# Performance work log

Hardware: AMD Instinct MI355X
Metric: run time of the kernel (lower is better)

## Reference

```python
import jax, jax.numpy as jnp
import numpy as np

B, TE, TD, E, H, V, A, MAXOOV = 8, 400, 100, 128, 256, 50000, 612, 50
VEXT = V + MAXOOV


def setup_inputs():
    key = jax.random.key(0)
    it = iter(jax.random.split(key, 40))
    def nrm(shape, s=0.05):
        return jax.random.normal(next(it), shape, jnp.float32) * s
    inp = {
        "encoder_tokens": jax.random.randint(next(it), (B, TE), 0, V, dtype=jnp.int32),
        "decoder_tokens": jax.random.randint(next(it), (B, TD), 0, V, dtype=jnp.int32),
        "encoder_ext_tokens": jax.random.randint(next(it), (B, TE), 0, VEXT, dtype=jnp.int32),
        "encoder_mask": jnp.ones((B, TE), jnp.float32),
        "embedding": nrm((V, E)),
        "Wih_f": nrm((E, 4 * H)), "Whh_f": nrm((H, 4 * H)), "b_f": jnp.zeros((4 * H,), jnp.float32),
        "Wih_b": nrm((E, 4 * H)), "Whh_b": nrm((H, 4 * H)), "b_b": jnp.zeros((4 * H,), jnp.float32),
        "Wred": nrm((2 * H, H)), "bred": jnp.zeros((H,), jnp.float32),
        "Wenc_feat": nrm((2 * H, A)), "benc_feat": jnp.zeros((A,), jnp.float32),
        "v": nrm((A,), 1.0),
        "Wx": nrm((E + 2 * H, E)), "bx": jnp.zeros((E,), jnp.float32),
        "Wih_d": nrm((E, 4 * H)), "Whh_d": nrm((H, 4 * H)), "b_d": jnp.zeros((4 * H,), jnp.float32),
        "Wdf": nrm((TD, 2 * H, A)), "bdf": jnp.zeros((TD, A), jnp.float32),
        "Wpg": nrm((2 * H + H + H + E, 1)), "bpg": jnp.zeros((1,), jnp.float32),
        "Wout": nrm((H + 2 * H, H)), "bout": jnp.zeros((H,), jnp.float32),
        "Wv": nrm((H, V)), "bv": jnp.zeros((V,), jnp.float32),
    }
    return inp


def _lstm(xs, Wih, Whh, b):
    # xs: [T, B, E] -> outputs [T, B, H], final (h, c)
    def step(carry, x):
        h, c = carry
        g = x @ Wih + h @ Whh + b
        i, f, gg, o = jnp.split(g, 4, axis=-1)  # torch gate order i,f,g,o
        c = jax.nn.sigmoid(f) * c + jax.nn.sigmoid(i) * jnp.tanh(gg)
        h = jax.nn.sigmoid(o) * jnp.tanh(c)
        return (h, c), h
    z = jnp.zeros((xs.shape[1], Whh.shape[0]), xs.dtype)
    (hT, cT), hs = jax.lax.scan(step, (z, z), xs)
    return hs, hT, cT


def reference(encoder_tokens, decoder_tokens, encoder_ext_tokens, encoder_mask,
              embedding, Wih_f, Whh_f, b_f, Wih_b, Whh_b, b_b, Wred, bred,
              Wenc_feat, benc_feat, v, Wx, bx, Wih_d, Whh_d, b_d, Wdf, bdf,
              Wpg, bpg, Wout, bout, Wv, bv):
    # ---- bidirectional LSTM encoder (full-length sequences, mask == 1) ----
    enc_emb = embedding[encoder_tokens]               # [B, TE, E]
    xs = enc_emb.transpose(1, 0, 2)                   # [TE, B, E]
    hf, hTf, cTf = _lstm(xs, Wih_f, Whh_f, b_f)
    hb_rev, hTb, cTb = _lstm(xs[::-1], Wih_b, Whh_b, b_b)
    hb = hb_rev[::-1]
    enc_out = jnp.concatenate([hf, hb], -1).transpose(1, 0, 2)  # [B, TE, 2H]

    # ---- state reducer (original uses reduce_h_layer for BOTH h and c) ----
    h0 = jax.nn.relu(jnp.concatenate([hTf, hTb], -1) @ Wred + bred)
    c0 = jax.nn.relu(jnp.concatenate([cTf, cTb], -1) @ Wred + bred)

    # ---- 1x1 conv == linear on encoder states ----
    enc_feat = enc_out @ Wenc_feat + benc_feat        # [B, TE, A]

    dec_emb = embedding[decoder_tokens].transpose(1, 0, 2)  # [TD, B, E]

    def dec_step(carry, xs_t):
        h, c, ctx = carry
        emb_t, Wdf_t, bdf_t = xs_t
        x = jnp.concatenate([emb_t, ctx], -1) @ Wx + bx          # [B, E]
        g = x @ Wih_d + h @ Whh_d + b_d
        i, f, gg, o = jnp.split(g, 4, axis=-1)
        c = jax.nn.sigmoid(f) * c + jax.nn.sigmoid(i) * jnp.tanh(gg)
        h = jax.nn.sigmoid(o) * jnp.tanh(c)
        dec_feat = jnp.concatenate([h, c], -1) @ Wdf_t + bdf_t   # [B, A] (per-step weights)
        e = jnp.einsum('a,bta->bt', v, jnp.tanh(enc_feat + dec_feat[:, None, :]))
        attn = jax.nn.softmax(e, axis=-1) * encoder_mask
        attn = attn / attn.sum(-1, keepdims=True)
        ctx = jnp.einsum('bt,btd->bd', attn, enc_out)            # [B, 2H]
        p_gen = jax.nn.sigmoid(jnp.concatenate([ctx, h, c, x], -1) @ Wpg + bpg)  # [B, 1]
        out = jnp.concatenate([h, ctx], -1) @ Wout + bout        # [B, H]
        return (h, c, ctx), (out, attn, p_gen)

    ctx0 = jnp.zeros((enc_out.shape[0], 2 * H), enc_out.dtype)
    _, (outs, attns, pgens) = jax.lax.scan(dec_step, (h0, c0, ctx0), (dec_emb, Wdf, bdf))
    # outs [TD,B,H], attns [TD,B,TE], pgens [TD,B,1]

    # ---- pointer-generator mixture over extended vocab ----
    vocab_dist = jax.nn.softmax(outs @ Wv + bv, axis=-1)         # [TD, B, V]
    vocab_dist = pgens * vocab_dist
    attn_w = (1.0 - pgens) * attns                               # [TD, B, TE]

    def scatter_one(a, idx):
        return jnp.zeros((VEXT,), a.dtype).at[idx].add(a)
    copy_dist = jax.vmap(jax.vmap(scatter_one, in_axes=(0, 0)), in_axes=(0, None))(
        attn_w, encoder_ext_tokens)                              # [TD, B, VEXT]

    extra = jnp.zeros(vocab_dist.shape[:2] + (MAXOOV,), vocab_dist.dtype)
    final = jnp.concatenate([vocab_dist, extra], -1) + copy_dist # [TD, B, VEXT]
    return final
```

## Files before the change

kernel.cpp:

```cpp
#include <hip/hip_runtime.h>

#define DEVI __device__ __forceinline__

constexpr int B_ = 8, TE_ = 400, TD_ = 100, E_ = 128, H_ = 256;
constexpr int A_ = 612, V_ = 50000, VEXT_ = 50050;
constexpr int H4_ = 1024, H2_ = 512;
constexpr int NS_ = 16, SLW_ = 40;

constexpr size_t OFS_HBF  = 0;
constexpr size_t OFS_HBB  = 4096;
constexpr size_t OFS_CT   = 8192;
constexpr size_t OFS_CHC  = 12288;
constexpr size_t OFS_PG   = 32896;
constexpr size_t OFS_SROW = 33696;
constexpr size_t OFS_FLG  = 34496;
constexpr size_t OFS_ATT  = 35520;
constexpr size_t OFS_EO   = 355520;
constexpr size_t OFS_OUTS = OFS_EO;
constexpr size_t OFS_EF   = OFS_EO + (size_t)B_*TE_*H2_;

constexpr size_t DO_GINF = 0;
constexpr size_t DO_GINB = DO_GINF + (size_t)TE_*B_*H4_;
constexpr size_t DO_GDEC = 2ull*(size_t)TE_*B_*H4_;
constexpr size_t DO_XPRE = DO_GDEC + (size_t)TD_*B_*H4_;
constexpr size_t DO_CTXH = DO_XPRE + (size_t)TD_*B_*E_;
constexpr size_t DO_HCH  = DO_CTXH + (size_t)TD_*B_*H2_;
constexpr size_t DO_WCG  = DO_HCH + (size_t)TD_*B_*H2_;
constexpr size_t DO_EOWT = DO_WCG + (size_t)H2_*H4_;
constexpr size_t DO_EPB  = DO_EOWT + (size_t)B_*H4_*TE_;

#if defined(__has_builtin)
#if __has_builtin(__builtin_amdgcn_rcpf)
#define HAS_RCPF 1
#endif
#endif

DEVI float rcp_fast(float x) {
#ifdef HAS_RCPF
  return __builtin_amdgcn_rcpf(x);
#else
  return 1.0f / x;
#endif
}

DEVI float sigm(float x) { return rcp_fast(1.0f + __expf(-x)); }
DEVI float tanh_fast(float x) {
  float e = __expf(2.0f * x);
  return 1.0f - 2.0f * rcp_fast(e + 1.0f);
}

DEVI float ld_at(const float* p) {
  unsigned u = __hip_atomic_load((const unsigned*)p, __ATOMIC_RELAXED, __HIP_MEMORY_SCOPE_AGENT);
  return __uint_as_float(u);
}
DEVI void st_at(float* p, float v) {
  __hip_atomic_store((unsigned*)p, __float_as_uint(v), __ATOMIC_RELAXED, __HIP_MEMORY_SCOPE_AGENT);
}

#define WAIT_VM() do { asm volatile("s_waitcnt vmcnt(0)" ::: "memory"); \
                       __builtin_amdgcn_sched_barrier(0); } while (0)

DEVI float wave_max(float v) {
#pragma unroll
  for (int o = 32; o; o >>= 1) v = fmaxf(v, __shfl_xor(v, o));
  return v;
}
DEVI float wave_sum(float v) {
#pragma unroll
  for (int o = 32; o; o >>= 1) v += __shfl_xor(v, o);
  return v;
}

DEVI void flag_bar(unsigned* flags, int ncheck, int slot, unsigned ep, int stride) {
  __syncthreads();
  if (threadIdx.x == 0) {
    asm volatile("s_waitcnt vmcnt(0)" ::: "memory");
    __hip_atomic_store(&flags[slot * stride], ep, __ATOMIC_RELAXED, __HIP_MEMORY_SCOPE_AGENT);
  }
  if ((int)threadIdx.x < ncheck) {
    while (__hip_atomic_load(&flags[threadIdx.x * stride], __ATOMIC_RELAXED,
                             __HIP_MEMORY_SCOPE_AGENT) < ep) {
      __builtin_amdgcn_s_sleep(2);
    }
  }
  __syncthreads();
  asm volatile("" ::: "memory");
}

__global__ __launch_bounds__(256) void k0_wcg(
    const float* __restrict__ Wx, const float* __restrict__ Wih_d,
    float* __restrict__ dob, float* __restrict__ ws)
{
  __shared__ float AsT[32 * 64];
  __shared__ float Bsh[32 * 64];
  const float* Am = Wx + 128 * 128;
  float* C = dob + DO_WCG;
  const int ct = blockIdx.x, rt = blockIdx.y, tid = threadIdx.x;
  if (ct == 0 && rt == 0) {
    for (int i = tid; i < 8192; i += 256) ws[OFS_HBF + i] = 0.0f;
    unsigned* f = (unsigned*)(ws + OFS_FLG);
    for (int i = tid; i < 1024; i += 256) f[i] = 0u;
  }
  const int c0 = ct * 64, r0 = rt * 64;
  const int tx = tid & 15, ty = tid >> 4;
  float4 acc0 = make_float4(0,0,0,0), acc1 = acc0, acc2 = acc0, acc3 = acc0;
  for (int kc = 0; kc < 4; ++kc) {
#pragma unroll
    for (int i = 0; i < 2; ++i) {
      int q = tid * 2 + i;
      int r = q >> 3, kq = q & 7;
      float4 v = *(const float4*)&Am[(size_t)(r0 + r) * 128 + kc * 32 + kq * 4];
      AsT[(kq * 4 + 0) * 64 + r] = v.x; AsT[(kq * 4 + 1) * 64 + r] = v.y;
      AsT[(kq * 4 + 2) * 64 + r] = v.z; AsT[(kq * 4 + 3) * 64 + r] = v.w;
    }
#pragma unroll
    for (int i = 0; i < 2; ++i) {
      int q = tid * 2 + i;
      int kk = q >> 4, cq = q & 15;
      *(float4*)&Bsh[kk * 64 + cq * 4] =
          *(const float4*)&Wih_d[(size_t)(kc * 32 + kk) * H4_ + c0 + cq * 4];
    }
    __syncthreads();
#pragma unroll
    for (int kk = 0; kk < 32; ++kk) {
      float4 w4 = *(float4*)&Bsh[kk * 64 + tx * 4];
      const float* ar = &AsT[kk * 64 + ty * 4];
      acc0.x += ar[0]*w4.x; acc0.y += ar[0]*w4.y; acc0.z += ar[0]*w4.z; acc0.w += ar[0]*w4.w;
      acc1.x += ar[1]*w4.x; acc1.y += ar[1]*w4.y; acc1.z += ar[1]*w4.z; acc1.w += ar[1]*w4.w;
      acc2.x += ar[2]*w4.x; acc2.y += ar[2]*w4.y; acc2.z += ar[2]*w4.z; acc2.w += ar[2]*w4.w;
      acc3.x += ar[3]*w4.x; acc3.y += ar[3]*w4.y; acc3.z += ar[3]*w4.z; acc3.w += ar[3]*w4.w;
    }
    __syncthreads();
  }
  float4 r4[4] = {acc0, acc1, acc2, acc3};
#pragma unroll
  for (int i = 0; i < 4; ++i)
    *(float4*)&C[(size_t)(r0 + ty * 4 + i) * H4_ + c0 + tx * 4] = r4[i];
}

__global__ __launch_bounds__(256) void k1_embed_gates(
    const int* __restrict__ etok, const float* __restrict__ emb,
    const float* __restrict__ Wih_f, const float* __restrict__ b_f,
    const float* __restrict__ Wih_b, const float* __restrict__ b_b,
    float* __restrict__ gin_f, float* __restrict__ gin_b)
{
  __shared__ float er[8 * 128];
  const int t = blockIdx.x, tid = threadIdx.x;
  for (int i = tid; i < 1024; i += 256) {
    int b = i >> 7, e = i & 127;
    er[i] = emb[(size_t)etok[b * TE_ + t] * E_ + e];
  }
  __syncthreads();
  float bfv[4], bbv[4];
#pragma unroll
  for (int g = 0; g < 4; ++g) { bfv[g] = b_f[g * H_ + tid]; bbv[g] = b_b[g * H_ + tid]; }
  float af[32], ab[32];
#pragma unroll
  for (int i = 0; i < 32; ++i) { af[i] = bfv[i & 3]; ab[i] = bbv[i & 3]; }
  for (int e = 0; e < E_; ++e) {
    float wf[4], wb[4];
#pragma unroll
    for (int g = 0; g < 4; ++g) {
      wf[g] = Wih_f[(size_t)e * H4_ + g * H_ + tid];
      wb[g] = Wih_b[(size_t)e * H4_ + g * H_ + tid];
    }
#pragma unroll
    for (int b = 0; b < 8; ++b) {
      float x = er[b * 128 + e];
#pragma unroll
      for (int g = 0; g < 4; ++g) { af[b * 4 + g] += x * wf[g]; ab[b * 4 + g] += x * wb[g]; }
    }
  }
#pragma unroll
  for (int b = 0; b < 8; ++b)
#pragma unroll
    for (int g = 0; g < 4; ++g) {
      gin_f[((size_t)t * 8 + b) * H4_ + g * H_ + tid] = af[b * 4 + g];
      gin_b[((size_t)t * 8 + b) * H4_ + g * H_ + tid] = ab[b * 4 + g];
    }
}

__global__ __launch_bounds__(256) void k1d_dec_pre(
    const int* __restrict__ dtok, const float* __restrict__ emb,
    const float* __restrict__ Wx, const float* __restrict__ bx,
    const float* __restrict__ Wih_d, const float* __restrict__ b_d,
    float* __restrict__ dob)
{
  __shared__ float er[8 * 128];
  __shared__ float xl[8 * 128];
  const int t = blockIdx.x, tid = threadIdx.x;
  for (int i = tid; i < 1024; i += 256) {
    int b = i >> 7, e = i & 127;
    er[i] = emb[(size_t)dtok[b * TD_ + t] * E_ + e];
  }
  __syncthreads();
  {
    const int col = tid & 127, bh = tid >> 7;
#pragma unroll
    for (int ii = 0; ii < 4; ++ii) {
      int b = bh + (ii << 1);
      float acc = bx[col];
      for (int k = 0; k < 128; ++k) acc += er[b * 128 + k] * Wx[(size_t)k * E_ + col];
      xl[b * 128 + col] = acc;
      dob[DO_XPRE + ((size_t)t * 8 + b) * E_ + col] = acc;
    }
  }
  __syncthreads();
  float bv[4];
#pragma unroll
  for (int g = 0; g < 4; ++g) bv[g] = b_d[g * H_ + tid];
  float af[32];
#pragma unroll
  for (int i = 0; i < 32; ++i) af[i] = bv[i & 3];
  for (int e = 0; e < E_; ++e) {
    float w[4];
#pragma unroll
    for (int g = 0; g < 4; ++g) w[g] = Wih_d[(size_t)e * H4_ + g * H_ + tid];
#pragma unroll
    for (int b = 0; b < 8; ++b) {
      float x = xl[b * 128 + e];
#pragma unroll
      for (int g = 0; g < 4; ++g) af[b * 4 + g] += x * w[g];
    }
  }
#pragma unroll
  for (int b = 0; b < 8; ++b)
#pragma unroll
    for (int g = 0; g < 4; ++g)
      dob[DO_GDEC + ((size_t)t * 8 + b) * H4_ + g * H_ + tid] = af[b * 4 + g];
}

__global__ __launch_bounds__(256, 1) void k2_encoder_scan(
    const float* __restrict__ gin_f, const float* __restrict__ gin_b,
    const float* __restrict__ Whh_f, const float* __restrict__ Whh_b,
    float* __restrict__ ws)
{
  __shared__ float sm[4096];
  const int bid = blockIdx.x, tid = threadIdx.x;
  const int dir = bid >> 5, c0 = (bid & 31) * 8;
  const float* Whh = dir ? Whh_b : Whh_f;
  const float* gin = dir ? gin_b : gin_f;
  float* hb = ws + (dir ? OFS_HBB : OFS_HBF);
  float* cT = ws + OFS_CT;
  float* eo = ws + OFS_EO;
  unsigned* flg = (unsigned*)(ws + OFS_FLG) + (dir ? 128 : 0);
  const int slot = bid & 31;

  const int jl = tid >> 3, kg = tid & 7;
  const int gt = jl >> 3, hcl = jl & 7;
  const int jcol = gt * H_ + c0 + hcl;
  float wreg[32];
#pragma unroll
  for (int kk = 0; kk < 32; ++kk) wreg[kk] = Whh[(size_t)(kg + kk * 8) * H4_ + jcol];

  const int uhc = tid >> 3, ub = tid & 7;
  float c_reg = 0.0f;
  unsigned ep = 0;

  for (int t = 0; t < TE_; ++t) {
    const int te = dir ? (TE_ - 1 - t) : t;
    float* hrd = hb + (t & 1) * 2048;
    float* hwr = hb + ((t & 1) ^ 1) * 2048;
    float gpre[4] = {0, 0, 0, 0};
    if (tid < 64) {
#pragma unroll
      for (int gg = 0; gg < 4; ++gg)
        gpre[gg] = gin[((size_t)te * 8 + ub) * H4_ + gg * H_ + c0 + uhc];
    }
    {
      float4 v0, v1;
      const float* a0 = &hrd[tid * 8];
      const float* a1 = &hrd[tid * 8 + 4];
      asm volatile(
          "global_load_dwordx4 %0, %2, off sc0 sc1\n\t"
          "global_load_dwordx4 %1, %3, off sc0 sc1"
          : "=&v"(v0), "=&v"(v1) : "v"(a0), "v"(a1));
      WAIT_VM();
      *(float4*)&sm[tid * 8] = v0;
      *(float4*)&sm[tid * 8 + 4] = v1;
    }
    __syncthreads();
    float acc[8] = {0, 0, 0, 0, 0, 0, 0, 0};
#pragma unroll
    for (int kk = 0; kk < 32; ++kk) {
      float w = wreg[kk];
      const float* hp = &sm[(kg + kk * 8) * 8];
#pragma unroll
      for (int b = 0; b < 8; ++b) acc[b] += hp[b] * w;
    }
    float* part = sm + 2048;
    *(float4*)&part[(jl * 8 + kg) * 8]     = make_float4(acc[0], acc[1], acc[2], acc[3]);
    *(float4*)&part[(jl * 8 + kg) * 8 + 4] = make_float4(acc[4], acc[5], acc[6], acc[7]);
    __syncthreads();
    if (tid < 64) {
      float g[4];
#pragma unroll
      for (int gg = 0; gg < 4; ++gg) {
        float s = gpre[gg];
#pragma unroll
        for (int k2 = 0; k2 < 8; ++k2) s += part[((gg * 8 + uhc) * 8 + k2) * 8 + ub];
        g[gg] = s;
      }
      float ci = sigm(g[0]), cf = sigm(g[1]), cg = tanh_fast(g[2]), co = sigm(g[3]);
      c_reg = cf * c_reg + ci * cg;
      float hn = co * tanh_fast(c_reg);
      st_at(&hwr[(c0 + uhc) * 8 + ub], hn);
      eo[((size_t)ub * TE_ + te) * H2_ + dir * H_ + c0 + uhc] = hn;
      if (t == TE_ - 1) cT[ub * H2_ + dir * H_ + c0 + uhc] = c_reg;
    }
    ep++; flag_bar(flg, 32, slot, ep, 4);
  }
}

__global__ __launch_bounds__(256) void k3_encfeat(
    const float* __restrict__ eo, const float* __restrict__ Wef,
    const float* __restrict__ bef, float* __restrict__ ef)
{
  __shared__ float AsT[32 * 64];
  __shared__ float Wsh[32 * 64];
  const int ct = blockIdx.x, rt = blockIdx.y, tid = threadIdx.x;
  const int c0 = ct * 64, r0 = rt * 64;
  const int tx = tid & 15, ty = tid >> 4;
  float4 acc0 = make_float4(0,0,0,0), acc1 = acc0, acc2 = acc0, acc3 = acc0;
  for (int kc = 0; kc < 16; ++kc) {
#pragma unroll
    for (int i = 0; i < 2; ++i) {
      int q = tid * 2 + i;
      int r = q >> 3, kq = q & 7;
      float4 v = *(const float4*)&eo[(size_t)(r0 + r) * H2_ + kc * 32 + kq * 4];
      AsT[(kq * 4 + 0) * 64 + r] = v.x; AsT[(kq * 4 + 1) * 64 + r] = v.y;
      AsT[(kq * 4 + 2) * 64 + r] = v.z; AsT[(kq * 4 + 3) * 64 + r] = v.w;
    }
#pragma unroll
    for (int i = 0; i < 2; ++i) {
      int q = tid * 2 + i;
      int kk = q >> 4, cq = q & 15;
      int col = c0 + cq * 4;
      float4 v = make_float4(0,0,0,0);
      if (col < A_) v = *(const float4*)&Wef[(size_t)(kc * 32 + kk) * A_ + col];
      *(float4*)&Wsh[kk * 64 + cq * 4] = v;
    }
    __syncthreads();
#pragma unroll
    for (int kk = 0; kk < 32; ++kk) {
      float4 w4 = *(float4*)&Wsh[kk * 64 + tx * 4];
      const float* ar = &AsT[kk * 64 + ty * 4];
      acc0.x += ar[0]*w4.x; acc0.y += ar[0]*w4.y; acc0.z += ar[0]*w4.z; acc0.w += ar[0]*w4.w;
      acc1.x += ar[1]*w4.x; acc1.y += ar[1]*w4.y; acc1.z += ar[1]*w4.z; acc1.w += ar[1]*w4.w;
      acc2.x += ar[2]*w4.x; acc2.y += ar[2]*w4.y; acc2.z += ar[2]*w4.z; acc2.w += ar[2]*w4.w;
      acc3.x += ar[3]*w4.x; acc3.y += ar[3]*w4.y; acc3.z += ar[3]*w4.z; acc3.w += ar[3]*w4.w;
    }
    __syncthreads();
  }
  const int col = c0 + tx * 4;
  if (col < A_) {
    float4 bb = *(const float4*)&bef[col];
    float4 r4[4] = {acc0, acc1, acc2, acc3};
#pragma unroll
    for (int i = 0; i < 4; ++i) {
      int row = r0 + ty * 4 + i;
      float4 o = make_float4(r4[i].x + bb.x, r4[i].y + bb.y, r4[i].z + bb.z, r4[i].w + bb.w);
      *(float4*)&ef[(size_t)row * A_ + col] = o;
    }
  }
}

__global__ __launch_bounds__(256) void k3b_eowt(
    const float* __restrict__ eo, const float* __restrict__ dob_c, float* __restrict__ dob)
{
  __shared__ float Wt[32 * 64];
  __shared__ float Et[32 * 40];
  const float* Wcg = dob_c + DO_WCG;
  float* eoWT = dob + DO_EOWT;
  const int jt = blockIdx.x, tt = blockIdx.y, b = blockIdx.z, tid = threadIdx.x;
  const int j0 = jt * 64, te0 = tt * 40;
  const int j_l = tid & 63, tq = tid >> 6;
  float acc[10];
#pragma unroll
  for (int u = 0; u < 10; ++u) acc[u] = 0.0f;
  for (int kc = 0; kc < 16; ++kc) {
#pragma unroll
    for (int i = 0; i < 2; ++i) {
      int q = tid * 2 + i;
      int kk = q >> 4, j4 = q & 15;
      *(float4*)&Wt[kk * 64 + j4 * 4] =
          *(const float4*)&Wcg[(size_t)(kc * 32 + kk) * H4_ + j0 + j4 * 4];
    }
#pragma unroll
    for (int i = 0; i < 2; ++i) {
      int q = tid + i * 256;
      if (q < 320) {
        int te_l = q >> 3, kq = q & 7;
        float4 v = *(const float4*)&eo[((size_t)b * TE_ + te0 + te_l) * H2_ + kc * 32 + kq * 4];
        Et[(kq * 4 + 0) * 40 + te_l] = v.x; Et[(kq * 4 + 1) * 40 + te_l] = v.y;
        Et[(kq * 4 + 2) * 40 + te_l] = v.z; Et[(kq * 4 + 3) * 40 + te_l] = v.w;
      }
    }
    __syncthreads();
#pragma unroll
    for (int kk = 0; kk < 32; ++kk) {
      float w = Wt[kk * 64 + j_l];
      const float* ep2 = &Et[kk * 40 + tq * 10];
#pragma unroll
      for (int u = 0; u < 10; ++u) acc[u] += w * ep2[u];
    }
    __syncthreads();
  }
  float* outp = &eoWT[((size_t)b * H4_ + j0 + j_l) * TE_ + te0 + tq * 10];
#pragma unroll
  for (int u = 0; u < 10; ++u) outp[u] = acc[u];
}

__global__ __launch_bounds__(512, 1) void k4_decoder(
    const float* __restrict__ maskp,
    const float* __restrict__ Wred, const float* __restrict__ bred,
    const float* __restrict__ Whh_d,
    const float* __restrict__ Wdf, const float* __restrict__ bdf,
    const float* __restrict__ vvec, float* __restrict__ ws, float* __restrict__ dob)
{
  __shared__ float eoW[TE_ * 64];
  __shared__ float eu[TE_];
  __shared__ float hcL[512];
  __shared__ float red[16];
  __shared__ float gdL[64];
  __shared__ float gl[64];
  __shared__ float pgl[64 * 9];
  __shared__ float prt[1280];
  __shared__ float dfl[48];
  __shared__ float bdfL[48];
  __shared__ float vvL[48];

  float* chc = ws + OFS_CHC;
  float* att = ws + OFS_ATT;
  const float* efG = ws + OFS_EF;
  const float* hbf = ws + OFS_HBF;
  const float* hbb = ws + OFS_HBB;
  const float* cT  = ws + OFS_CT;
  unsigned* flgF = (unsigned*)(ws + OFS_FLG) + 256;
  const float* gdec = dob + DO_GDEC;
  const float* eoWT = dob + DO_EOWT;
  float* epb = dob + DO_EPB;
  float* hch = dob + DO_HCH;
  const int bid = blockIdx.x, tid = threadIdx.x;
  const int b = bid >> 4, s = bid & 15;
  unsigned* flgG = (unsigned*)(ws + OFS_FLG) + 512 + b * 64;
  const int a0 = s * SLW_, w = (s == 15) ? 12 : SLW_;
  const int nq = w >> 2;

  for (int i = tid; i < 64 * 100; i += 512) {
    int jgi = i / 100, c = i - jgi * 100;
    int jreal = (jgi >> 4) * 256 + s * 16 + (jgi & 15);
    float4 v = *(const float4*)&eoWT[((size_t)b * H4_ + jreal) * TE_ + c * 4];
    eoW[(c * 4 + 0) * 64 + jgi] = v.x;
    eoW[(c * 4 + 1) * 64 + jgi] = v.y;
    eoW[(c * 4 + 2) * 64 + jgi] = v.z;
    eoW[(c * 4 + 3) * 64 + jgi] = v.w;
  }
  const int jg = tid & 63, l8 = tid >> 6;
  const int jreal = (jg >> 4) * 256 + s * 16 + (jg & 15);
  float wreg[32];
#pragma unroll
  for (int kk = 0; kk < 32; ++kk)
    wreg[kk] = Whh_d[(size_t)(l8 + kk * 8) * H4_ + jreal];
  if (tid < w) vvL[tid] = vvec[a0 + tid];

  if (bid < 32) {
    const int isC = bid >> 4, pb = (bid >> 1) & 7, half = bid & 1;
    if (tid < 512)
      hcL[tid] = isC ? cT[pb * H2_ + tid]
                     : (tid < H_ ? hbf[tid * 8 + pb] : hbb[(tid - H_) * 8 + pb]);
    __syncthreads();
    {
      const int col_l = tid & 127, ks = tid >> 7;
      float acc = 0.0f;
      for (int kk = 0; kk < 128; ++kk) {
        int k = ks * 128 + kk;
        acc += hcL[k] * Wred[(size_t)k * H_ + half * 128 + col_l];
      }
      prt[ks * 128 + col_l] = acc;
    }
    __syncthreads();
    if (tid < 128) {
      float v2 = fmaxf(prt[tid] + prt[128 + tid] + prt[256 + tid] + prt[384 + tid] +
                       bred[half * 128 + tid], 0.0f);
      st_at(&chc[pb * H2_ + isC * H_ + half * 128 + tid], v2);
    }
  } else {
    float dm = 0.0f;
#pragma unroll
    for (int i = 0; i < 7; ++i) {
      int f = (bid - 32) * 3264 + i * 512 + tid;
      if (i * 512 + tid < 3264 && f < H2_ * A_) dm += Wdf[f];
    }
    asm volatile("" :: "v"(dm));
  }
  unsigned ep = 1;
  flag_bar(flgF, 128, bid, ep, 2);

  float c_reg = 0.0f;
  if (tid < 16) c_reg = ld_at(&chc[b * H2_ + H_ + s * 16 + tid]);
  unsigned epg = 0;

  for (int t = 0; t <= TD_; ++t) {
    const int cur = t & 1, nxt = cur ^ 1;

    {
      const int teA = (tid < TE_) ? tid : TE_ - 1;
      const int tcl = (t < TD_) ? t : TD_ - 1;
      const float* ae = &epb[((size_t)b * TE_ + teA) * 16];
      const float* ah = &chc[cur * 4096 + b * H2_ + (tid & 63) * 4];
      const int gi = tid & 15;
      const float* agd = &gdec[((size_t)tcl * 8 + b) * H4_ +
                               (gi >> 2) * 256 + s * 16 + (gi & 3) * 4];
      float4 v0, v1, v2, v3, vh, vgd;
      asm volatile(
          "global_load_dwordx4 %0, %6, off sc0 sc1\n\t"
          "global_load_dwordx4 %1, %7, off sc0 sc1\n\t"
          "global_load_dwordx4 %2, %8, off sc0 sc1\n\t"
          "global_load_dwordx4 %3, %9, off sc0 sc1\n\t"
          "global_load_dwordx4 %4, %10, off sc0 sc1\n\t"
          "global_load_dwordx4 %5, %11, off sc0 sc1"
          : "=&v"(v0), "=&v"(v1), "=&v"(v2), "=&v"(v3), "=&v"(vh), "=&v"(vgd)
          : "v"(ae), "v"(ae + 4), "v"(ae + 8), "v"(ae + 12), "v"(ah), "v"(agd));
      WAIT_VM();
      if (t > 0 && tid < TE_)
        eu[tid] = (v0.x + v0.y + v0.z + v0.w) + (v1.x + v1.y + v1.z + v1.w) +
                  (v2.x + v2.y + v2.z + v2.w) + (v3.x + v3.y + v3.z + v3.w);
      if (tid < 64) *(float4*)&hcL[tid * 4] = vh;
      if (tid < 16) *(float4*)&gdL[(gi >> 2) * 16 + (gi & 3) * 4] = vgd;
      __syncthreads();

      float inv = 0.0f;
      if (t > 0) {
        float m = (tid < TE_) ? eu[tid] : -3.4e38f;
        m = wave_max(m);
        if ((tid & 63) == 0) red[tid >> 6] = m;
        __syncthreads();
        m = red[0];
#pragma unroll
        for (int i = 1; i < 8; ++i) m = fmaxf(m, red[i]);
        float u = 0.0f;
        if (tid < TE_) {
          u = __expf(eu[tid] - m) * maskp[b * TE_ + tid];
          eu[tid] = u;
        }
        float sl = wave_sum(u);
        if ((tid & 63) == 0) red[8 + (tid >> 6)] = sl;
        __syncthreads();
        float S = 0.0f;
#pragma unroll
        for (int i = 0; i < 8; ++i) S += red[8 + i];
        inv = rcp_fast(S);
      }

      if (t > 0 && tid < 25)
        att[((size_t)(t - 1) * 8 + b) * TE_ + s * 25 + tid] = eu[s * 25 + tid] * inv;

      if (t < TD_) {
        float accG = 0.0f, accW = 0.0f;
        if (t > 0) {
          for (int te = l8; te < TE_; te += 8)
            accG += eoW[te * 64 + jg] * eu[te];
        }
#pragma unroll
        for (int kk = 0; kk < 32; ++kk)
          accW += wreg[kk] * hcL[l8 + kk * 8];
        pgl[jg * 9 + l8] = accG * inv + accW;
        __syncthreads();
        if (tid < 64) {
          float sg = gdL[tid];
#pragma unroll
          for (int l = 0; l < 8; ++l) sg += pgl[tid * 9 + l];
          gl[tid] = sg;
        }
        __syncthreads();
        if (tid < 16) {
          float g0 = gl[tid], g1 = gl[16 + tid], g2 = gl[32 + tid], g3 = gl[48 + tid];
          float ci = sigm(g0), cf = sigm(g1), cg = tanh_fast(g2), co = sigm(g3);
          c_reg = cf * c_reg + ci * cg;
          float hn = co * tanh_fast(c_reg);
          int hc = s * 16 + tid;
          st_at(&chc[nxt * 4096 + b * H2_ + hc], hn);
          st_at(&chc[nxt * 4096 + b * H2_ + H_ + hc], c_reg);
          hch[((size_t)t * 8 + b) * H2_ + hc] = hn;
          hch[((size_t)t * 8 + b) * H2_ + H_ + hc] = c_reg;
        }
      }
    }
    if (t == TD_) break;
    epg++; flag_bar(flgG, 16, s, epg, 4);

    {
      {
        const float* ahc = &chc[nxt * 4096 + b * H2_ + (tid & 127) * 4];
        const int cl = (tid < 10) ? tid : 9;
        const float* abf = &bdf[(size_t)t * A_ + a0 + cl * 4];
        float4 vhc, vbf;
        asm volatile(
            "global_load_dwordx4 %0, %2, off sc0 sc1\n\t"
            "global_load_dwordx4 %1, %3, off sc0 sc1"
            : "=&v"(vhc), "=&v"(vbf) : "v"(ahc), "v"(abf));
        WAIT_VM();
        if (tid < 128) *(float4*)&hcL[tid * 4] = vhc;
        if (tid < 10) *(float4*)&bdfL[tid * 4] = vbf;
      }
      __syncthreads();

      const float* wp = Wdf + (size_t)t * H2_ * A_;
      {
        const int kq = tid >> 4, al = tid & 15;
        if (al < nq) {
          float4 a4 = make_float4(0, 0, 0, 0);
          const float* wpc = wp + a0 + al * 4;
#pragma unroll
          for (int i = 0; i < 16; ++i) {
            int k = kq * 16 + i;
            float4 w4 = *(const float4*)&wpc[(size_t)k * A_];
            float hv = hcL[k];
            a4.x += hv * w4.x; a4.y += hv * w4.y; a4.z += hv * w4.z; a4.w += hv * w4.w;
          }
          *(float4*)&prt[(kq * 10 + al) * 4] = a4;
        }
      }
      float dm = 0.0f;
      if (t + 1 < TD_) {
        const float* wp1 = Wdf + (size_t)(t + 1) * H2_ * A_;
#pragma unroll
        for (int q = 0; q < 2; ++q) {
          int f = tid + q * 512;
          if (f < 640) {
            int r = f / 10, c4 = f - r * 10;
            if (c4 < nq) {
              float4 vx = *(const float4*)&wp1[(size_t)(b * 64 + r) * A_ + a0 + c4 * 4];
              dm += vx.x + vx.y + vx.z + vx.w;
            }
          }
        }
      }
      __syncthreads();
      if (tid < w) {
        float ssum = bdfL[tid];
        const int c4 = tid >> 2, r = tid & 3;
#pragma unroll
        for (int kq = 0; kq < 32; ++kq) ssum += prt[(kq * 10 + c4) * 4 + r];
        dfl[tid] = ssum;
      }
      __syncthreads();

      if (tid < TE_) {
        const float* efp = &efG[((size_t)b * TE_ + tid) * A_ + a0];
        float acc = 0.0f;
        for (int q = 0; q < nq; ++q) {
          float4 e4 = *(const float4*)&efp[q * 4];
          const float* dd = &dfl[q * 4];
          const float* vv = &vvL[q * 4];
          acc += vv[0] * tanh_fast(e4.x + dd[0]);
          acc += vv[1] * tanh_fast(e4.y + dd[1]);
          acc += vv[2] * tanh_fast(e4.z + dd[2]);
          acc += vv[3] * tanh_fast(e4.w + dd[3]);
        }
        st_at(&epb[((size_t)b * TE_ + tid) * 16 + s], acc);
      }
      asm volatile("" :: "v"(dm));
    }
    epg++; flag_bar(flgG, 16, s, epg, 4);
  }
}

__global__ __launch_bounds__(256) void k4c_ctx(
    const float* __restrict__ ws, float* __restrict__ dob)
{
  __shared__ float AsT[32 * 64];
  __shared__ float Bsh[32 * 64];
  const float* att = ws + OFS_ATT;
  const float* eo  = ws + OFS_EO;
  float* ctxh = dob + DO_CTXH;
  const int ct = blockIdx.x, rt = blockIdx.y, b = blockIdx.z, tid = threadIdx.x;
  const int c0 = ct * 64, r0 = rt * 64;
  const int tx = tid & 15, ty = tid >> 4;
  float4 acc0 = make_float4(0,0,0,0), acc1 = acc0, acc2 = acc0, acc3 = acc0;
  for (int kc = 0; kc < 13; ++kc) {
#pragma unroll
    for (int i = 0; i < 2; ++i) {
      int q = tid * 2 + i;
      int r = q >> 3, kq = q & 7;
      int k = kc * 32 + kq * 4;
      float4 v = make_float4(0, 0, 0, 0);
      if (k < TE_ && r0 + r < TD_)
        v = *(const float4*)&att[((size_t)(r0 + r) * 8 + b) * TE_ + k];
      AsT[(kq * 4 + 0) * 64 + r] = v.x; AsT[(kq * 4 + 1) * 64 + r] = v.y;
      AsT[(kq * 4 + 2) * 64 + r] = v.z; AsT[(kq * 4 + 3) * 64 + r] = v.w;
    }
#pragma unroll
    for (int i = 0; i < 2; ++i) {
      int q = tid * 2 + i;
      int kk = q >> 4, cq = q & 15;
      int k = kc * 32 + kk;
      float4 v = make_float4(0, 0, 0, 0);
      if (k < TE_) v = *(const float4*)&eo[((size_t)b * TE_ + k) * H2_ + c0 + cq * 4];
      *(float4*)&Bsh[kk * 64 + cq * 4] = v;
    }
    __syncthreads();
#pragma unroll
    for (int kk = 0; kk < 32; ++kk) {
      float4 w4 = *(float4*)&Bsh[kk * 64 + tx * 4];
      const float* ar = &AsT[kk * 64 + ty * 4];
      acc0.x += ar[0]*w4.x; acc0.y += ar[0]*w4.y; acc0.z += ar[0]*w4.z; acc0.w += ar[0]*w4.w;
      acc1.x += ar[1]*w4.x; acc1.y += ar[1]*w4.y; acc1.z += ar[1]*w4.z; acc1.w += ar[1]*w4.w;
      acc2.x += ar[2]*w4.x; acc2.y += ar[2]*w4.y; acc2.z += ar[2]*w4.z; acc2.w += ar[2]*w4.w;
      acc3.x += ar[3]*w4.x; acc3.y += ar[3]*w4.y; acc3.z += ar[3]*w4.z; acc3.w += ar[3]*w4.w;
    }
    __syncthreads();
  }
  float4 r4[4] = {acc0, acc1, acc2, acc3};
#pragma unroll
  for (int i = 0; i < 4; ++i) {
    int row = r0 + ty * 4 + i;
    if (row < TD_)
      *(float4*)&ctxh[((size_t)row * 8 + b) * H2_ + c0 + tx * 4] = r4[i];
  }
}

__global__ __launch_bounds__(256) void k4b_post(
    const float* __restrict__ Wx, const float* __restrict__ Wout, const float* __restrict__ bout,
    const float* __restrict__ Wpg, const float* __restrict__ bpg,
    float* __restrict__ ws, const float* __restrict__ dob)
{
  __shared__ float hcl[4096], ctxl[4096], cpl[4096], xl[1024], red2[256];
  const int t = blockIdx.x, tid = threadIdx.x;
  const float* hch  = dob + DO_HCH;
  const float* ctxh = dob + DO_CTXH;
  const float* xpre = dob + DO_XPRE;
  for (int i = tid; i < 4096; i += 256) {
    hcl[i]  = hch[(size_t)t * 4096 + i];
    ctxl[i] = ctxh[(size_t)t * 4096 + i];
    cpl[i]  = t ? ctxh[(size_t)(t - 1) * 4096 + i] : 0.0f;
  }
  __syncthreads();
  {
    const int col = tid & 127, bh = tid >> 7;
#pragma unroll
    for (int ii = 0; ii < 4; ++ii) {
      int b = bh + (ii << 1);
      float acc = xpre[(size_t)t * 1024 + b * E_ + col];
      for (int k = 0; k < H2_; ++k) acc += cpl[b * H2_ + k] * Wx[(size_t)(128 + k) * E_ + col];
      xl[b * E_ + col] = acc;
    }
  }
  __syncthreads();
  {
    const int col = tid;
    for (int b = 0; b < 8; ++b) {
      float acc = bout[col];
      for (int k = 0; k < 768; ++k)
        acc += (k < H_ ? hcl[b * H2_ + k] : ctxl[b * H2_ + (k - H_)]) * Wout[(size_t)k * H_ + col];
      ws[OFS_OUTS + ((size_t)t * 8 + b) * H_ + col] = acc;
    }
  }
  {
    const int b = tid >> 5, sg = tid & 31;
    float acc = 0.0f;
    for (int j = 0; j < 36; ++j) {
      int k = sg * 36 + j;
      float xv;
      if (k < H2_)       xv = ctxl[b * H2_ + k];
      else if (k < 768)  xv = hcl[b * H2_ + (k - H2_)];
      else if (k < 1024) xv = hcl[b * H2_ + H_ + (k - 768)];
      else               xv = xl[b * E_ + (k - 1024)];
      acc += xv * Wpg[k];
    }
    red2[tid] = acc;
    __syncthreads();
    if (tid < 8) {
      float s = 0.0f;
      for (int k2 = 0; k2 < 32; ++k2) s += red2[tid * 32 + k2];
      ws[OFS_PG + t * 8 + tid] = sigm(s + bpg[0]);
    }
  }
}

__global__ __launch_bounds__(256) void k5a_logits(
    const float* __restrict__ outs, const float* __restrict__ Wv,
    const float* __restrict__ bv, float* __restrict__ out)
{
  __shared__ float aT[32 * 64];
  __shared__ float wl[32 * 256];
  const int rt = blockIdx.x, ct = blockIdx.y, tid = threadIdx.x;
  const int r0 = rt * 64, c0 = ct * 256;
  const int cq = tid & 63, rg = tid >> 6;
  float4 acc[16];
#pragma unroll
  for (int i = 0; i < 16; ++i) acc[i] = make_float4(0, 0, 0, 0);
  for (int kc = 0; kc < 8; ++kc) {
#pragma unroll
    for (int i = 0; i < 2; ++i) {
      int q = tid * 2 + i;
      int r = q >> 3, kq = q & 7;
      float4 v = make_float4(0, 0, 0, 0);
      if (r0 + r < 800) v = *(const float4*)&outs[(size_t)(r0 + r) * H_ + kc * 32 + kq * 4];
      aT[(kq * 4 + 0) * 64 + r] = v.x; aT[(kq * 4 + 1) * 64 + r] = v.y;
      aT[(kq * 4 + 2) * 64 + r] = v.z; aT[(kq * 4 + 3) * 64 + r] = v.w;
    }
#pragma unroll
    for (int i = 0; i < 8; ++i) {
      int q = tid + i * 256;
      int kk = q >> 6, c4 = q & 63;
      int col = c0 + c4 * 4;
      float4 v = make_float4(0, 0, 0, 0);
      if (col < V_) v = *(const float4*)&Wv[(size_t)(kc * 32 + kk) * V_ + col];
      *(float4*)&wl[kk * 256 + c4 * 4] = v;
    }
    __syncthreads();
#pragma unroll
    for (int kk = 0; kk < 32; ++kk) {
      float4 w4 = *(float4*)&wl[kk * 256 + cq * 4];
      const float* ar = &aT[kk * 64 + rg * 16];
#pragma unroll
      for (int rr = 0; rr < 16; ++rr) {
        float a = ar[rr];
        acc[rr].x += a * w4.x; acc[rr].y += a * w4.y;
        acc[rr].z += a * w4.z; acc[rr].w += a * w4.w;
      }
    }
    __syncthreads();
  }
  const int col = c0 + cq * 4;
  if (col < V_) {
    float4 bb = *(const float4*)&bv[col];
#pragma unroll
    for (int rr = 0; rr < 16; ++rr) {
      int row = r0 + rg * 16 + rr;
      if (row < 800) {
        float2 lo = make_float2(acc[rr].x + bb.x, acc[rr].y + bb.y);
        float2 hi = make_float2(acc[rr].z + bb.z, acc[rr].w + bb.w);
        *(float2*)&out[(size_t)row * VEXT_ + col] = lo;
        *(float2*)&out[(size_t)row * VEXT_ + col + 2] = hi;
      }
    }
  }
}

__global__ __launch_bounds__(256) void k5b_rowsum(const float* __restrict__ out, float* __restrict__ Srow)
{
  __shared__ float red[256];
  const int r = blockIdx.x, tid = threadIdx.x;
  const float* base = out + (size_t)r * VEXT_;
  float s = 0.0f;
  for (int i = tid; i < V_ / 2; i += 256) {
    float2 v = *(const float2*)&base[i * 2];
    s += __expf(v.x) + __expf(v.y);
  }
  red[tid] = s; __syncthreads();
  for (int st = 128; st > 0; st >>= 1) { if (tid < st) red[tid] += red[tid + st]; __syncthreads(); }
  if (tid == 0) Srow[r] = red[0];
}

__global__ __launch_bounds__(256) void k5c_final(
    float* __restrict__ out, const float* __restrict__ Srow, const float* __restrict__ pg)
{
  const int cc = blockIdx.x, r = blockIdx.y, tid = threadIdx.x;
  const float scale = pg[r] * rcp_fast(Srow[r]);
  float* base = out + (size_t)r * VEXT_;
#pragma unroll
  for (int i = 0; i < 4; ++i) {
    int col = cc * 2048 + i * 512 + tid * 2;
    if (col < V_) {
      float2 v = *(float2*)&base[col];
      v.x = __expf(v.x) * scale; v.y = __expf(v.y) * scale;
      *(float2*)&base[col] = v;
    } else if (col < VEXT_) {
      *(float2*)&base[col] = make_float2(0.0f, 0.0f);
    }
  }
}

__global__ __launch_bounds__(256) void k5d_scatter(
    float* __restrict__ out, const float* __restrict__ ws, const int* __restrict__ ext)
{
  const int r = blockIdx.x, tid = threadIdx.x;
  const int b = r & 7;
  const float* at = ws + OFS_ATT + (size_t)r * TE_;
  const float w = 1.0f - ws[OFS_PG + r];
  float* base = out + (size_t)r * VEXT_;
  for (int i = tid; i < TE_; i += 256)
    atomicAdd(&base[ext[b * TE_ + i]], w * at[i]);
}

extern "C" void kernel_launch(void* const* d_in, const int* in_sizes, int n_in,
                              void* d_out, int out_size, void* d_ws, size_t ws_size,
                              hipStream_t stream) {
  const int*   etok  = (const int*)d_in[0];
  const int*   dtok  = (const int*)d_in[1];
  const int*   ext   = (const int*)d_in[2];
  const float* maskp = (const float*)d_in[3];
  const float* emb   = (const float*)d_in[4];
  const float* Wih_f = (const float*)d_in[5];
  const float* Whh_f = (const float*)d_in[6];
  const float* b_f   = (const float*)d_in[7];
  const float* Wih_b = (const float*)d_in[8];
  const float* Whh_b = (const float*)d_in[9];
  const float* b_b   = (const float*)d_in[10];
  const float* Wred  = (const float*)d_in[11];
  const float* bred  = (const float*)d_in[12];
  const float* Wef   = (const float*)d_in[13];
  const float* bef   = (const float*)d_in[14];
  const float* vvec  = (const float*)d_in[15];
  const float* Wx    = (const float*)d_in[16];
  const float* bx    = (const float*)d_in[17];
  const float* Wih_d = (const float*)d_in[18];
  const float* Whh_d = (const float*)d_in[19];
  const float* b_d   = (const float*)d_in[20];
  const float* Wdf   = (const float*)d_in[21];
  const float* bdf   = (const float*)d_in[22];
  const float* Wpg   = (const float*)d_in[23];
  const float* bpg   = (const float*)d_in[24];
  const float* Wout  = (const float*)d_in[25];
  const float* bout  = (const float*)d_in[26];
  const float* Wv    = (const float*)d_in[27];
  const float* bv    = (const float*)d_in[28];
  float* out = (float*)d_out;
  float* wsf = (float*)d_ws;
  float* dob = out;

  float* gin_f = dob + DO_GINF;
  float* gin_b = dob + DO_GINB;

  k0_wcg<<<dim3(16, 8), 256, 0, stream>>>(Wx, Wih_d, dob, wsf);
  k1_embed_gates<<<400, 256, 0, stream>>>(etok, emb, Wih_f, b_f, Wih_b, b_b, gin_f, gin_b);
  k1d_dec_pre<<<100, 256, 0, stream>>>(dtok, emb, Wx, bx, Wih_d, b_d, dob);

  {
    void* args2[5] = {(void*)&gin_f, (void*)&gin_b, (void*)&Whh_f, (void*)&Whh_b, (void*)&wsf};
    if (hipLaunchCooperativeKernel((void*)k2_encoder_scan, dim3(64), dim3(256), args2, 0, stream) != hipSuccess)
      k2_encoder_scan<<<64, 256, 0, stream>>>(gin_f, gin_b, Whh_f, Whh_b, wsf);
  }

  k3_encfeat<<<dim3(10, 50), 256, 0, stream>>>(wsf + OFS_EO, Wef, bef, wsf + OFS_EF);
  k3b_eowt<<<dim3(16, 10, 8), 256, 0, stream>>>(wsf + OFS_EO, dob, dob);

  {
    void* args4[9] = {(void*)&maskp, (void*)&Wred, (void*)&bred, (void*)&Whh_d,
                      (void*)&Wdf, (void*)&bdf, (void*)&vvec, (void*)&wsf, (void*)&dob};
    if (hipLaunchCooperativeKernel((void*)k4_decoder, dim3(128), dim3(512), args4, 0, stream) != hipSuccess)
      k4_decoder<<<128, 512, 0, stream>>>(maskp, Wred, bred, Whh_d, Wdf, bdf, vvec, wsf, dob);
  }

  k4c_ctx<<<dim3(8, 2, 8), 256, 0, stream>>>(wsf, dob);
  k4b_post<<<100, 256, 0, stream>>>(Wx, Wout, bout, Wpg, bpg, wsf, dob);

  k5a_logits<<<dim3(13, 196), 256, 0, stream>>>(wsf + OFS_OUTS, Wv, bv, out);
  k5b_rowsum<<<800, 256, 0, stream>>>(out, wsf + OFS_SROW);
  k5c_final<<<dim3(25, 800), 256, 0, stream>>>(out, wsf + OFS_SROW, wsf + OFS_PG);
  k5d_scatter<<<800, 256, 0, stream>>>(out, wsf, ext);
}
```

Before: 3.555 ms.

## Split decoder across 32 slices per batch and cache encoder features in LDS

The cooperative decoder kernel grows from 128 to 256 blocks, so each batch row is split into 32 slices instead of 16. Each block then owns 8 gate columns and about 19-20 attention features, which shrinks per-step work and register use. Each block's slice of the encoder feature matrix is preloaded into shared memory once instead of being re-read from global memory every step. The trade-off is that each per-step barrier now waits on twice as many blocks, the epb partial-sum reads double, the flag region grows, and the flag check becomes an equality test.

```diff
diff --git a/kernel.cpp b/kernel.cpp
--- a/kernel.cpp
+++ b/kernel.cpp
@@ -5,7 +5,6 @@
 constexpr int B_ = 8, TE_ = 400, TD_ = 100, E_ = 128, H_ = 256;
 constexpr int A_ = 612, V_ = 50000, VEXT_ = 50050;
 constexpr int H4_ = 1024, H2_ = 512;
-constexpr int NS_ = 16, SLW_ = 40;
 
 constexpr size_t OFS_HBF  = 0;
 constexpr size_t OFS_HBB  = 4096;
@@ -14,8 +13,8 @@
 constexpr size_t OFS_PG   = 32896;
 constexpr size_t OFS_SROW = 33696;
 constexpr size_t OFS_FLG  = 34496;
-constexpr size_t OFS_ATT  = 35520;
-constexpr size_t OFS_EO   = 355520;
+constexpr size_t OFS_ATT  = 36544;
+constexpr size_t OFS_EO   = 356544;
 constexpr size_t OFS_OUTS = OFS_EO;
 constexpr size_t OFS_EF   = OFS_EO + (size_t)B_*TE_*H2_;
 
@@ -79,7 +78,7 @@
   }
   if ((int)threadIdx.x < ncheck) {
     while (__hip_atomic_load(&flags[threadIdx.x * stride], __ATOMIC_RELAXED,
-                             __HIP_MEMORY_SCOPE_AGENT) < ep) {
+                             __HIP_MEMORY_SCOPE_AGENT) != ep) {
       __builtin_amdgcn_s_sleep(2);
     }
   }
@@ -99,7 +98,7 @@
   if (ct == 0 && rt == 0) {
     for (int i = tid; i < 8192; i += 256) ws[OFS_HBF + i] = 0.0f;
     unsigned* f = (unsigned*)(ws + OFS_FLG);
-    for (int i = tid; i < 1024; i += 256) f[i] = 0u;
+    for (int i = tid; i < 2048; i += 256) f[i] = 0u;
   }
   const int c0 = ct * 64, r0 = rt * 64;
   const int tx = tid & 15, ty = tid >> 4;
@@ -418,17 +417,18 @@
     const float* __restrict__ Wdf, const float* __restrict__ bdf,
     const float* __restrict__ vvec, float* __restrict__ ws, float* __restrict__ dob)
 {
-  __shared__ float eoW[TE_ * 64];
+  __shared__ float eoW[TE_ * 32];
+  __shared__ float efL[TE_ * 20];
   __shared__ float eu[TE_];
   __shared__ float hcL[512];
   __shared__ float red[16];
-  __shared__ float gdL[64];
-  __shared__ float gl[64];
-  __shared__ float pgl[64 * 9];
-  __shared__ float prt[1280];
-  __shared__ float dfl[48];
-  __shared__ float bdfL[48];
-  __shared__ float vvL[48];
+  __shared__ float gdL[32];
+  __shared__ float gl[32];
+  __shared__ float pgl[32 * 17];
+  __shared__ float prt[512];
+  __shared__ float dfl[20];
+  __shared__ float bdfL[20];
+  __shared__ float vvL[20];
 
   float* chc = ws + OFS_CHC;
   float* att = ws + OFS_ATT;
@@ -442,26 +442,26 @@
   float* epb = dob + DO_EPB;
   float* hch = dob + DO_HCH;
   const int bid = blockIdx.x, tid = threadIdx.x;
-  const int b = bid >> 4, s = bid & 15;
-  unsigned* flgG = (unsigned*)(ws + OFS_FLG) + 512 + b * 64;
-  const int a0 = s * SLW_, w = (s == 15) ? 12 : SLW_;
-  const int nq = w >> 2;
-
-  for (int i = tid; i < 64 * 100; i += 512) {
+  const int b = bid >> 5, s = bid & 31;
+  unsigned* flgG = (unsigned*)(ws + OFS_FLG) + 768 + b * 128;
+  const int a0 = (s < 4) ? s * 20 : 80 + (s - 4) * 19;
+  const int w  = (s < 4) ? 20 : 19;
+
+  for (int i = tid; i < 32 * 100; i += 512) {
     int jgi = i / 100, c = i - jgi * 100;
-    int jreal = (jgi >> 4) * 256 + s * 16 + (jgi & 15);
+    int jreal = (jgi >> 3) * 256 + s * 8 + (jgi & 7);
     float4 v = *(const float4*)&eoWT[((size_t)b * H4_ + jreal) * TE_ + c * 4];
-    eoW[(c * 4 + 0) * 64 + jgi] = v.x;
-    eoW[(c * 4 + 1) * 64 + jgi] = v.y;
-    eoW[(c * 4 + 2) * 64 + jgi] = v.z;
-    eoW[(c * 4 + 3) * 64 + jgi] = v.w;
-  }
-  const int jg = tid & 63, l8 = tid >> 6;
-  const int jreal = (jg >> 4) * 256 + s * 16 + (jg & 15);
-  float wreg[32];
-#pragma unroll
-  for (int kk = 0; kk < 32; ++kk)
-    wreg[kk] = Whh_d[(size_t)(l8 + kk * 8) * H4_ + jreal];
+    eoW[(c * 4 + 0) * 32 + jgi] = v.x;
+    eoW[(c * 4 + 1) * 32 + jgi] = v.y;
+    eoW[(c * 4 + 2) * 32 + jgi] = v.z;
+    eoW[(c * 4 + 3) * 32 + jgi] = v.w;
+  }
+  const int jg = tid >> 4, l16 = tid & 15;
+  const int jreal = (jg >> 3) * 256 + s * 8 + (jg & 7);
+  float wreg[16];
+#pragma unroll
+  for (int kk = 0; kk < 16; ++kk)
+    wreg[kk] = Whh_d[(size_t)(l16 + kk * 16) * H4_ + jreal];
   if (tid < w) vvL[tid] = vvec[a0 + tid];
 
   if (bid < 32) {
@@ -485,20 +485,27 @@
                        bred[half * 128 + tid], 0.0f);
       st_at(&chc[pb * H2_ + isC * H_ + half * 128 + tid], v2);
     }
+    __syncthreads();
   } else {
+    const int p = bid - 32;
     float dm = 0.0f;
-#pragma unroll
-    for (int i = 0; i < 7; ++i) {
-      int f = (bid - 32) * 3264 + i * 512 + tid;
-      if (i * 512 + tid < 3264 && f < H2_ * A_) dm += Wdf[f];
+    {
+      int base = p * 350;
+      if (tid < 350 && base + tid < 78336) {
+        float4 vx = ((const float4*)Wdf)[base + tid];
+        dm += vx.x + vx.y + vx.z + vx.w;
+      }
     }
     asm volatile("" :: "v"(dm));
   }
-  unsigned ep = 1;
-  flag_bar(flgF, 128, bid, ep, 2);
+  for (int i = tid; i < 8000; i += 512) {
+    int te = i / 20, c = i - te * 20;
+    efL[i] = (c < w) ? efG[((size_t)b * TE_ + te) * A_ + a0 + c] : 0.0f;
+  }
+  flag_bar(flgF, 256, bid, 1, 2);
 
   float c_reg = 0.0f;
-  if (tid < 16) c_reg = ld_at(&chc[b * H2_ + H_ + s * 16 + tid]);
+  if (tid < 8) c_reg = ld_at(&chc[b * H2_ + H_ + s * 8 + tid]);
   unsigned epg = 0;
 
   for (int t = 0; t <= TD_; ++t) {
@@ -507,12 +514,12 @@
     {
       const int teA = (tid < TE_) ? tid : TE_ - 1;
       const int tcl = (t < TD_) ? t : TD_ - 1;
-      const float* ae = &epb[((size_t)b * TE_ + teA) * 16];
+      const float* ae = &epb[((size_t)b * TE_ + teA) * 32];
       const float* ah = &chc[cur * 4096 + b * H2_ + (tid & 63) * 4];
-      const int gi = tid & 15;
+      const int gi = tid & 7;
       const float* agd = &gdec[((size_t)tcl * 8 + b) * H4_ +
-                               (gi >> 2) * 256 + s * 16 + (gi & 3) * 4];
-      float4 v0, v1, v2, v3, vh, vgd;
+                               (gi >> 1) * 256 + s * 8 + (gi & 1) * 4];
+      float4 e0, e1, e2, e3, e4, e5, e6, e7, vh, vgd;
       asm volatile(
           "global_load_dwordx4 %0, %6, off sc0 sc1\n\t"
           "global_load_dwordx4 %1, %7, off sc0 sc1\n\t"
@@ -520,14 +527,23 @@
           "global_load_dwordx4 %3, %9, off sc0 sc1\n\t"
           "global_load_dwordx4 %4, %10, off sc0 sc1\n\t"
           "global_load_dwordx4 %5, %11, off sc0 sc1"
-          : "=&v"(v0), "=&v"(v1), "=&v"(v2), "=&v"(v3), "=&v"(vh), "=&v"(vgd)
-          : "v"(ae), "v"(ae + 4), "v"(ae + 8), "v"(ae + 12), "v"(ah), "v"(agd));
+          : "=&v"(e0), "=&v"(e1), "=&v"(e2), "=&v"(e3), "=&v"(e4), "=&v"(e5)
+          : "v"(ae), "v"(ae + 4), "v"(ae + 8), "v"(ae + 12), "v"(ae + 16), "v"(ae + 20));
+      asm volatile(
+          "global_load_dwordx4 %0, %4, off sc0 sc1\n\t"
+          "global_load_dwordx4 %1, %5, off sc0 sc1\n\t"
+          "global_load_dwordx4 %2, %6, off sc0 sc1\n\t"
+          "global_load_dwordx4 %3, %7, off sc0 sc1"
+          : "=&v"(e6), "=&v"(e7), "=&v"(vh), "=&v"(vgd)
+          : "v"(ae + 24), "v"(ae + 28), "v"(ah), "v"(agd));
       WAIT_VM();
       if (t > 0 && tid < TE_)
-        eu[tid] = (v0.x + v0.y + v0.z + v0.w) + (v1.x + v1.y + v1.z + v1.w) +
-                  (v2.x + v2.y + v2.z + v2.w) + (v3.x + v3.y + v3.z + v3.w);
+        eu[tid] = (e0.x + e0.y + e0.z + e0.w) + (e1.x + e1.y + e1.z + e1.w) +
+                  (e2.x + e2.y + e2.z + e2.w) + (e3.x + e3.y + e3.z + e3.w) +
+                  (e4.x + e4.y + e4.z + e4.w) + (e5.x + e5.y + e5.z + e5.w) +
+                  (e6.x + e6.y + e6.z + e6.w) + (e7.x + e7.y + e7.z + e7.w);
       if (tid < 64) *(float4*)&hcL[tid * 4] = vh;
-      if (tid < 16) *(float4*)&gdL[(gi >> 2) * 16 + (gi & 3) * 4] = vgd;
+      if (tid < 8) *(float4*)&gdL[(gi >> 1) * 8 + (gi & 1) * 4] = vgd;
       __syncthreads();
 
       float inv = 0.0f;
@@ -553,33 +569,33 @@
         inv = rcp_fast(S);
       }
 
-      if (t > 0 && tid < 25)
+      if (t > 0 && s < 16 && tid < 25)
         att[((size_t)(t - 1) * 8 + b) * TE_ + s * 25 + tid] = eu[s * 25 + tid] * inv;
 
       if (t < TD_) {
         float accG = 0.0f, accW = 0.0f;
         if (t > 0) {
-          for (int te = l8; te < TE_; te += 8)
-            accG += eoW[te * 64 + jg] * eu[te];
+          for (int te = l16; te < TE_; te += 16)
+            accG += eoW[te * 32 + jg] * eu[te];
         }
 #pragma unroll
-        for (int kk = 0; kk < 32; ++kk)
-          accW += wreg[kk] * hcL[l8 + kk * 8];
-        pgl[jg * 9 + l8] = accG * inv + accW;
+        for (int kk = 0; kk < 16; ++kk)
+          accW += wreg[kk] * hcL[l16 + kk * 16];
+        pgl[jg * 17 + l16] = accG * inv + accW;
         __syncthreads();
-        if (tid < 64) {
+        if (tid < 32) {
           float sg = gdL[tid];
 #pragma unroll
-          for (int l = 0; l < 8; ++l) sg += pgl[tid * 9 + l];
+          for (int l = 0; l < 16; ++l) sg += pgl[tid * 17 + l];
           gl[tid] = sg;
         }
         __syncthreads();
-        if (tid < 16) {
-          float g0 = gl[tid], g1 = gl[16 + tid], g2 = gl[32 + tid], g3 = gl[48 + tid];
+        if (tid < 8) {
+          float g0 = gl[tid], g1 = gl[8 + tid], g2 = gl[16 + tid], g3 = gl[24 + tid];
           float ci = sigm(g0), cf = sigm(g1), cg = tanh_fast(g2), co = sigm(g3);
           c_reg = cf * c_reg + ci * cg;
           float hn = co * tanh_fast(c_reg);
-          int hc = s * 16 + tid;
+          int hc = s * 8 + tid;
           st_at(&chc[nxt * 4096 + b * H2_ + hc], hn);
           st_at(&chc[nxt * 4096 + b * H2_ + H_ + hc], c_reg);
           hch[((size_t)t * 8 + b) * H2_ + hc] = hn;
@@ -588,82 +604,59 @@
       }
     }
     if (t == TD_) break;
-    epg++; flag_bar(flgG, 16, s, epg, 4);
+    epg++; flag_bar(flgG, 32, s, epg, 4);
 
     {
       {
         const float* ahc = &chc[nxt * 4096 + b * H2_ + (tid & 127) * 4];
-        const int cl = (tid < 10) ? tid : 9;
-        const float* abf = &bdf[(size_t)t * A_ + a0 + cl * 4];
-        float4 vhc, vbf;
-        asm volatile(
-            "global_load_dwordx4 %0, %2, off sc0 sc1\n\t"
-            "global_load_dwordx4 %1, %3, off sc0 sc1"
-            : "=&v"(vhc), "=&v"(vbf) : "v"(ahc), "v"(abf));
+        float4 vhc;
+        asm volatile("global_load_dwordx4 %0, %1, off sc0 sc1" : "=&v"(vhc) : "v"(ahc));
+        if (tid < w) bdfL[tid] = bdf[(size_t)t * A_ + a0 + tid];
         WAIT_VM();
         if (tid < 128) *(float4*)&hcL[tid * 4] = vhc;
-        if (tid < 10) *(float4*)&bdfL[tid * 4] = vbf;
       }
       __syncthreads();
 
       const float* wp = Wdf + (size_t)t * H2_ * A_;
       {
-        const int kq = tid >> 4, al = tid & 15;
-        if (al < nq) {
-          float4 a4 = make_float4(0, 0, 0, 0);
-          const float* wpc = wp + a0 + al * 4;
-#pragma unroll
-          for (int i = 0; i < 16; ++i) {
-            int k = kq * 16 + i;
-            float4 w4 = *(const float4*)&wpc[(size_t)k * A_];
-            float hv = hcL[k];
-            a4.x += hv * w4.x; a4.y += hv * w4.y; a4.z += hv * w4.z; a4.w += hv * w4.w;
-          }
-          *(float4*)&prt[(kq * 10 + al) * 4] = a4;
-        }
-      }
-      float dm = 0.0f;
-      if (t + 1 < TD_) {
-        const float* wp1 = Wdf + (size_t)(t + 1) * H2_ * A_;
-#pragma unroll
-        for (int q = 0; q < 2; ++q) {
-          int f = tid + q * 512;
-          if (f < 640) {
-            int r = f / 10, c4 = f - r * 10;
-            if (c4 < nq) {
-              float4 vx = *(const float4*)&wp1[(size_t)(b * 64 + r) * A_ + a0 + c4 * 4];
-              dm += vx.x + vx.y + vx.z + vx.w;
-            }
+        const int kq = tid >> 5, col = tid & 31;
+        float acc = 0.0f;
+        if (col < w) {
+          const float* wpc = wp + a0 + col;
+#pragma unroll 8
+          for (int i = 0; i < 32; ++i) {
+            int k = kq * 32 + i;
+            acc += hcL[k] * wpc[(size_t)k * A_];
           }
         }
+        prt[col * 16 + kq] = acc;
+      }
+      float dm = 0.0f;
+      if (t + 1 < TD_ && tid < 192) {
+        const float* wp1 = Wdf + (size_t)(t + 1) * H2_ * A_;
+        int r = tid / 3, sel = tid - r * 3;
+        int c = (sel == 0) ? 0 : ((sel == 1) ? 16 : (w - 1));
+        if (c < w) dm += wp1[(size_t)(b * 64 + r) * A_ + a0 + c];
       }
       __syncthreads();
       if (tid < w) {
         float ssum = bdfL[tid];
-        const int c4 = tid >> 2, r = tid & 3;
-#pragma unroll
-        for (int kq = 0; kq < 32; ++kq) ssum += prt[(kq * 10 + c4) * 4 + r];
+#pragma unroll
+        for (int kq = 0; kq < 16; ++kq) ssum += prt[tid * 16 + kq];
         dfl[tid] = ssum;
       }
       __syncthreads();
 
       if (tid < TE_) {
-        const float* efp = &efG[((size_t)b * TE_ + tid) * A_ + a0];
+        const float* efp = &efL[tid * 20];
         float acc = 0.0f;
-        for (int q = 0; q < nq; ++q) {
-          float4 e4 = *(const float4*)&efp[q * 4];
-          const float* dd = &dfl[q * 4];
-          const float* vv = &vvL[q * 4];
-          acc += vv[0] * tanh_fast(e4.x + dd[0]);
-          acc += vv[1] * tanh_fast(e4.y + dd[1]);
-          acc += vv[2] * tanh_fast(e4.z + dd[2]);
-          acc += vv[3] * tanh_fast(e4.w + dd[3]);
-        }
-        st_at(&epb[((size_t)b * TE_ + tid) * 16 + s], acc);
+        for (int j = 0; j < w; ++j)
+          acc += vvL[j] * tanh_fast(efp[j] + dfl[j]);
+        st_at(&epb[((size_t)b * TE_ + tid) * 32 + s], acc);
       }
       asm volatile("" :: "v"(dm));
     }
-    epg++; flag_bar(flgG, 16, s, epg, 4);
+    epg++; flag_bar(flgG, 32, s, epg, 4);
   }
 }
 
@@ -941,8 +934,8 @@
   {
     void* args4[9] = {(void*)&maskp, (void*)&Wred, (void*)&bred, (void*)&Whh_d,
                       (void*)&Wdf, (void*)&bdf, (void*)&vvec, (void*)&wsf, (void*)&dob};
-    if (hipLaunchCooperativeKernel((void*)k4_decoder, dim3(128), dim3(512), args4, 0, stream) != hipSuccess)
-      k4_decoder<<<128, 512, 0, stream>>>(maskp, Wred, bred, Whh_d, Wdf, bdf, vvec, wsf, dob);
+    if (hipLaunchCooperativeKernel((void*)k4_decoder, dim3(256), dim3(512), args4, 0, stream) != hipSuccess)
+      k4_decoder<<<256, 512, 0, stream>>>(maskp, Wred, bred, Whh_d, Wdf, bdf, vvec, wsf, dob);
   }
 
   k4c_ctx<<<dim3(8, 2, 8), 256, 0, stream>>>(wsf, dob);
```

New measurement: 3.761 ms. +5.8%, slower.
